# Kernel tuning notes

Hardware: AMD Instinct MI355X
Metric: run time of the kernel (lower is better)

## Reference

```python
import jax, jax.numpy as jnp
import numpy as np

N_HEADS = 8
HIDDEN = 256
D_HEAD = HIDDEN // N_HEADS
N_NODES = 4096
N_EDGES = 16384


def setup_inputs() -> dict:
    key = jax.random.key(0)
    ks = jax.random.split(key, 12)
    s = 0.05
    return {
        "q": jax.random.normal(ks[0], (N_EDGES, HIDDEN), jnp.float32),
        "k": jax.random.normal(ks[1], (N_NODES, HIDDEN), jnp.float32),
        "v": jax.random.normal(ks[2], (N_NODES, HIDDEN), jnp.float32),
        "T": jax.random.uniform(ks[3], (N_NODES, N_EDGES), jnp.float32),
        "Wq": jax.random.normal(ks[4], (HIDDEN, HIDDEN), jnp.float32) * s,
        "bq": jax.random.normal(ks[5], (HIDDEN,), jnp.float32) * s,
        "Wk": jax.random.normal(ks[6], (HIDDEN, HIDDEN), jnp.float32) * s,
        "bk": jax.random.normal(ks[7], (HIDDEN,), jnp.float32) * s,
        "Wv": jax.random.normal(ks[8], (HIDDEN, HIDDEN), jnp.float32) * s,
        "bv": jax.random.normal(ks[9], (HIDDEN,), jnp.float32) * s,
        "Wo": jax.random.normal(ks[10], (HIDDEN, HIDDEN), jnp.float32) * s,
        "bo": jax.random.normal(ks[11], (HIDDEN,), jnp.float32) * s,
    }


def reference(q, k, v, T, Wq, bq, Wk, bk, Wv, bv, Wo, bo):
    scale = D_HEAD ** (-0.5)
    # projections, reshaped to per-head layout
    qh = (q @ Wq.T + bq).reshape(-1, N_HEADS, D_HEAD)  # [E, H, d]
    kh = (k @ Wk.T + bk).reshape(-1, N_HEADS, D_HEAD)  # [N, H, d]
    vh = (v @ Wv.T + bv).reshape(-1, N_HEADS, D_HEAD)  # [N, H, d]
    # row-normalized transition matrix (rows with zero sum left unscaled)
    row_sum = jnp.sum(T, axis=-1, keepdims=True)       # [N, 1]
    Tn = T / jnp.where(row_sum == 0, 1.0, row_sum)     # [N, E]
    # edge->node aggregation of queries, then scale
    qn = jnp.einsum("ne,ehd->nhd", Tn, qh) * scale     # [N, H, d]
    # attention: full NxN scores per head
    scores = jnp.einsum("nhd,mhd->hnm", qn, kh)        # [H, N, N]
    attn = jax.nn.softmax(scores, axis=-1)
    ctx = jnp.einsum("hnm,mhd->nhd", attn, vh)         # [N, H, d]
    out = ctx.reshape(-1, N_HEADS * D_HEAD) @ Wo.T + bo  # [N, hidden]
    return out
```

## Files before the change

kernel.cpp:

```cpp
#include <hip/hip_runtime.h>


#define N_NODES 4096
#define N_EDGES 16384
#define HIDDEN  256
#define KSPLIT  16

typedef __attribute__((ext_vector_type(4))) float f32x4;
typedef __attribute__((ext_vector_type(8))) short s16x8;
typedef __attribute__((ext_vector_type(4))) unsigned short u16x4;
typedef __attribute__((ext_vector_type(8))) unsigned short u16x8;

__device__ __forceinline__ unsigned short f2bf(float f) {
    union { float f; unsigned u; } x; x.f = f;
    unsigned r = x.u + 0x7FFFu + ((x.u >> 16) & 1u);
    return (unsigned short)(r >> 16);
}
__device__ __forceinline__ s16x8 pack8s(f32x4 x, f32x4 y) {
    u16x8 o;
    o[0]=f2bf(x[0]); o[1]=f2bf(x[1]); o[2]=f2bf(x[2]); o[3]=f2bf(x[3]);
    o[4]=f2bf(y[0]); o[5]=f2bf(y[1]); o[6]=f2bf(y[2]); o[7]=f2bf(y[3]);
    union { u16x8 u; s16x8 s; } c; c.u = o; return c.s;
}

__global__ __launch_bounds__(256)
void cvtW(const float* __restrict__ Wq, const float* __restrict__ Wk,
          const float* __restrict__ Wv, const float* __restrict__ Wo,
          unsigned short* __restrict__ dst)
{
    const int g = blockIdx.x * 256 + threadIdx.x;
    const long base = (long)g * 8;
    const int mat = (int)(base >> 16), off = (int)(base & 65535);
    const float* src = (mat == 0) ? Wq : (mat == 1) ? Wk : (mat == 2) ? Wv : Wo;
    f32x4 x = *(const f32x4*)&src[off];
    f32x4 y = *(const f32x4*)&src[off + 4];
    union { u16x8 u; s16x8 s; } c; c.s = pack8s(x, y);
    *(u16x8*)&dst[base] = c.u;
}

template<int MODE>
__global__ __launch_bounds__(256)
void proj_mfma(const float* __restrict__ A, const unsigned short* __restrict__ Wbf,
               const float* __restrict__ bias, unsigned short* __restrict__ out, int M)
{
    const int t = threadIdx.x;
    const int w = t >> 6, l = t & 63, lo = l & 15, h4 = l >> 4;
    const int m0 = blockIdx.x * 64 + w * 16;
    const int bn = blockIdx.y * 64;
    const float* Ar = A + (long)(m0 + lo) * 256 + h4 * 8;

    f32x4 acc[4] = {};
    #pragma unroll
    for (int kk = 0; kk < 8; ++kk) {
        f32x4 x = *(const f32x4*)&Ar[kk * 32];
        f32x4 y = *(const f32x4*)&Ar[kk * 32 + 4];
        s16x8 af = pack8s(x, y);
        #pragma unroll
        for (int nj = 0; nj < 4; ++nj) {
            s16x8 bf = *(const s16x8*)&Wbf[(bn + nj * 16 + lo) * 256 + kk * 32 + h4 * 8];
            acc[nj] = __builtin_amdgcn_mfma_f32_16x16x32_bf16(af, bf, acc[nj], 0, 0, 0);
        }
    }
    #pragma unroll
    for (int nj = 0; nj < 4; ++nj) {
        const int n = bn + nj * 16 + lo;
        const float bi = bias[n];
        if (MODE == 1) {
            #pragma unroll
            for (int r = 0; r < 4; ++r)
                out[(long)(m0 + h4 * 4 + r) * 256 + n] = f2bf(acc[nj][r] + bi);
        } else {
            u16x4 o;
            #pragma unroll
            for (int r = 0; r < 4; ++r) o[r] = f2bf(acc[nj][r] + bi);
            *(u16x4*)&out[(long)n * M + m0 + h4 * 4] = o;
        }
    }
}

__global__ __launch_bounds__(256)
void proj_out_mfma(const float* __restrict__ pctx, const float* __restrict__ plp,
                   const unsigned short* __restrict__ Wobf, const float* __restrict__ bo,
                   float* __restrict__ out)
{
    const int t = threadIdx.x;
    const int w = t >> 6, l = t & 63, lo = l & 15, h4 = l >> 4;
    const int m0 = blockIdx.x * 64 + w * 16;
    const int bn = blockIdx.y * 64;
    const int m = m0 + lo;

    float inv[8];
    #pragma unroll
    for (int h = 0; h < 8; ++h) {
        float s = plp[(0 * 8 + h) * N_NODES + m] + plp[(1 * 8 + h) * N_NODES + m]
                + plp[(2 * 8 + h) * N_NODES + m] + plp[(3 * 8 + h) * N_NODES + m];
        inv[h] = 1.0f / s;
    }
    const float* P = pctx + (long)m * 256;
    const long PS = (long)N_NODES * 256;

    f32x4 acc[4] = {};
    #pragma unroll
    for (int kk = 0; kk < 8; ++kk) {
        const int off = kk * 32 + h4 * 8;
        f32x4 x = *(const f32x4*)&P[off]          + *(const f32x4*)&P[PS + off]
                + *(const f32x4*)&P[2 * PS + off] + *(const f32x4*)&P[3 * PS + off];
        f32x4 y = *(const f32x4*)&P[off + 4]          + *(const f32x4*)&P[PS + off + 4]
                + *(const f32x4*)&P[2 * PS + off + 4] + *(const f32x4*)&P[3 * PS + off + 4];
        s16x8 af = pack8s(x * inv[kk], y * inv[kk]);
        #pragma unroll
        for (int nj = 0; nj < 4; ++nj) {
            s16x8 bf = *(const s16x8*)&Wobf[(bn + nj * 16 + lo) * 256 + kk * 32 + h4 * 8];
            acc[nj] = __builtin_amdgcn_mfma_f32_16x16x32_bf16(af, bf, acc[nj], 0, 0, 0);
        }
    }
    #pragma unroll
    for (int nj = 0; nj < 4; ++nj) {
        const int n = bn + nj * 16 + lo;
        const float bi = bo[n];
        #pragma unroll
        for (int r = 0; r < 4; ++r)
            out[(long)(m0 + h4 * 4 + r) * 256 + n] = acc[nj][r] + bi;
    }
}

__global__ __launch_bounds__(512, 4)
void tgemm(const float* __restrict__ T, const unsigned short* __restrict__ Bt,
           float* __restrict__ part, float* __restrict__ rsp)
{
    __shared__ __align__(16) unsigned short Bsm[2][256 * 64];
    const int t  = threadIdx.x;
    const int ks = blockIdx.x & 15, ms = blockIdx.x >> 4;
    const int m0 = ms * 128;
    const long k00 = (long)ks * 1024;
    const int w = t >> 6, l = t & 63, lo = l & 15, h4 = l >> 4;

    const int kx = ((l & 7) * 8) ^ ((l >> 3) << 3);
    const unsigned short* Bsrc = Bt + k00 + kx;

#define STAGE(itv, bufv) do {                                                       \
    const unsigned short* _s = Bsrc + (long)(itv) * 64;                             \
    unsigned short* _d = &Bsm[(bufv)][w * 2048];                                    \
    _Pragma("unroll")                                                               \
    for (int _i = 0; _i < 4; ++_i)                                                  \
        __builtin_amdgcn_global_load_lds(                                           \
            (const __attribute__((address_space(1))) unsigned int*)                 \
                (_s + (long)(w * 32 + _i * 8 + (l >> 3)) * N_EDGES),                \
            (__attribute__((address_space(3))) unsigned int*)(_d + _i * 512),       \
            16, 0, 0);                                                              \
} while (0)

    const float* Arow = T + (long)(m0 + w * 16 + lo) * N_EDGES + k00 + h4 * 8;

    STAGE(0, 0);
    f32x4 a0 = *(const f32x4*)&Arow[0];
    f32x4 a1 = *(const f32x4*)&Arow[4];
    f32x4 a2 = *(const f32x4*)&Arow[32];
    f32x4 a3 = *(const f32x4*)&Arow[36];
    __syncthreads();

    f32x4 acc[16] = {};
    float rs = 0.f;

    for (int it = 0; it < 16; ++it) {
        const int cur = it & 1;
        if (it < 15) STAGE(it + 1, cur ^ 1);
        s16x8 af0 = pack8s(a0, a1);
        s16x8 af1 = pack8s(a2, a3);
        rs += a0[0]+a0[1]+a0[2]+a0[3] + a1[0]+a1[1]+a1[2]+a1[3]
            + a2[0]+a2[1]+a2[2]+a2[3] + a3[0]+a3[1]+a3[2]+a3[3];
        if (it < 15) {
            const float* An = Arow + (it + 1) * 64;
            a0 = *(const f32x4*)&An[0];
            a1 = *(const f32x4*)&An[4];
            a2 = *(const f32x4*)&An[32];
            a3 = *(const f32x4*)&An[36];
        }
        const unsigned short* Bb = Bsm[cur];
        const int swz = (lo & 7) << 3;
        #pragma unroll
        for (int nj = 0; nj < 16; ++nj) {
            const int jb = (nj * 16 + lo) * 64;
            s16x8 bf0 = *(const s16x8*)&Bb[jb + ((h4 * 8) ^ swz)];
            s16x8 bf1 = *(const s16x8*)&Bb[jb + ((32 + h4 * 8) ^ swz)];
            acc[nj] = __builtin_amdgcn_mfma_f32_16x16x32_bf16(af0, bf0, acc[nj], 0, 0, 0);
            acc[nj] = __builtin_amdgcn_mfma_f32_16x16x32_bf16(af1, bf1, acc[nj], 0, 0, 0);
        }
        __syncthreads();
    }
#undef STAGE

    rs += __shfl_xor(rs, 16); rs += __shfl_xor(rs, 32);
    if (h4 == 0) rsp[ks * N_NODES + m0 + w * 16 + lo] = rs;

    float* P = part + (long)ks * (N_NODES * HIDDEN);
    #pragma unroll
    for (int nj = 0; nj < 16; ++nj)
        #pragma unroll
        for (int r = 0; r < 4; ++r)
            P[(long)(m0 + w * 16 + h4 * 4 + r) * HIDDEN + nj * 16 + lo] = acc[nj][r];
}

__global__ __launch_bounds__(256)
void finalize(const float* __restrict__ part, const float* __restrict__ rsp,
              unsigned short* __restrict__ qn)
{
    const int idx = blockIdx.x * 256 + threadIdx.x;
    const long i4 = (long)idx * 4;
    const int n = (int)(i4 >> 8);
    f32x4 s = {};
    #pragma unroll
    for (int ksp = 0; ksp < KSPLIT; ++ksp)
        s += *(const f32x4*)&part[(long)ksp * (N_NODES * HIDDEN) + i4];
    float rs = 0.f;
    #pragma unroll
    for (int ksp = 0; ksp < KSPLIT; ++ksp) rs += rsp[ksp * N_NODES + n];
    rs = (rs == 0.0f) ? 1.0f : rs;
    const float sc = 0.17677669529663687f / rs;
    u16x4 o;
    #pragma unroll
    for (int i = 0; i < 4; ++i) o[i] = f2bf(s[i] * sc);
    *(u16x4*)&qn[i4] = o;
}

__global__ __launch_bounds__(256)
void attn(const unsigned short* __restrict__ qn, const unsigned short* __restrict__ kh,
          const unsigned short* __restrict__ vht, float* __restrict__ pctx,
          float* __restrict__ plp)
{
    __shared__ __align__(16) unsigned short Ksm[64 * 40];
    __shared__ __align__(16) unsigned short Vsm[32 * 72];
    __shared__ __align__(16) unsigned short Psm[4][32 * 72];
    const int t  = threadIdx.x;
    const int hh = blockIdx.x >> 7, nb = (blockIdx.x >> 2) & 31, mh = blockIdx.x & 3;
    const int w = t >> 6, l = t & 63, lo = l & 15, h4 = l >> 4;
    const int n0 = nb * 128 + w * 32;

    const int km = t >> 2, kdc = (t & 3) * 8;
    const int vd = t >> 3, vmc = (t & 7) * 8;

    s16x8 qf[2];
    #pragma unroll
    for (int ni = 0; ni < 2; ++ni)
        qf[ni] = *(const s16x8*)&qn[(long)(n0 + ni * 16 + lo) * HIDDEN + hh * 32 + h4 * 8];

    f32x4 acc[2][2] = {};
    float lp[2][4] = {};
    const f32x4 zero = {};

    for (int mt = mh * 16; mt < mh * 16 + 16; ++mt) {
        const int m0 = mt * 64;
        *(s16x8*)&Ksm[km * 40 + kdc] =
            *(const s16x8*)&kh[(long)(m0 + km) * HIDDEN + hh * 32 + kdc];
        *(s16x8*)&Vsm[vd * 72 + vmc] =
            *(const s16x8*)&vht[(long)(hh * 32 + vd) * N_NODES + m0 + vmc];
        __syncthreads();

        s16x8 kb[4];
        #pragma unroll
        for (int mi = 0; mi < 4; ++mi)
            kb[mi] = *(const s16x8*)&Ksm[(mi * 16 + lo) * 40 + h4 * 8];
        #pragma unroll
        for (int ni = 0; ni < 2; ++ni) {
            #pragma unroll
            for (int mi = 0; mi < 4; ++mi) {
                f32x4 s = __builtin_amdgcn_mfma_f32_16x16x32_bf16(qf[ni], kb[mi], zero, 0, 0, 0);
                #pragma unroll
                for (int r = 0; r < 4; ++r) {
                    float p = __expf(s[r]);
                    lp[ni][r] += p;
                    Psm[w][(ni * 16 + h4 * 4 + r) * 72 + mi * 16 + lo] = f2bf(p);
                }
            }
        }
        s16x8 pa[2][2], vb[2][2];
        #pragma unroll
        for (int ni = 0; ni < 2; ++ni)
            #pragma unroll
            for (int k2 = 0; k2 < 2; ++k2)
                pa[ni][k2] = *(const s16x8*)&Psm[w][(ni * 16 + lo) * 72 + k2 * 32 + h4 * 8];
        #pragma unroll
        for (int di = 0; di < 2; ++di)
            #pragma unroll
            for (int k2 = 0; k2 < 2; ++k2)
                vb[di][k2] = *(const s16x8*)&Vsm[(di * 16 + lo) * 72 + k2 * 32 + h4 * 8];
        #pragma unroll
        for (int k2 = 0; k2 < 2; ++k2)
            #pragma unroll
            for (int ni = 0; ni < 2; ++ni)
                #pragma unroll
                for (int di = 0; di < 2; ++di)
                    acc[ni][di] = __builtin_amdgcn_mfma_f32_16x16x32_bf16(
                        pa[ni][k2], vb[di][k2], acc[ni][di], 0, 0, 0);
        __syncthreads();
    }
    #pragma unroll
    for (int ni = 0; ni < 2; ++ni)
        #pragma unroll
        for (int r = 0; r < 4; ++r) {
            float v2 = lp[ni][r];
            v2 += __shfl_xor(v2, 1); v2 += __shfl_xor(v2, 2);
            v2 += __shfl_xor(v2, 4); v2 += __shfl_xor(v2, 8);
            lp[ni][r] = v2;
        }
    float* myctx = pctx + (long)mh * (N_NODES * HIDDEN);
    float* myplp = plp  + (long)(mh * 8 + hh) * N_NODES;
    if (lo == 0)
        #pragma unroll
        for (int ni = 0; ni < 2; ++ni)
            #pragma unroll
            for (int r = 0; r < 4; ++r)
                myplp[n0 + ni * 16 + h4 * 4 + r] = lp[ni][r];
    #pragma unroll
    for (int ni = 0; ni < 2; ++ni)
        #pragma unroll
        for (int di = 0; di < 2; ++di)
            #pragma unroll
            for (int r = 0; r < 4; ++r)
                myctx[(long)(n0 + ni * 16 + h4 * 4 + r) * HIDDEN + hh * 32 + di * 16 + lo]
                    = acc[ni][di][r];
}

extern "C" void kernel_launch(void* const* d_in, const int* in_sizes, int n_in,
                              void* d_out, int out_size, void* d_ws, size_t ws_size,
                              hipStream_t stream)
{
    const float* q  = (const float*)d_in[0];
    const float* k  = (const float*)d_in[1];
    const float* v  = (const float*)d_in[2];
    const float* T  = (const float*)d_in[3];
    const float* Wq = (const float*)d_in[4];  const float* bq = (const float*)d_in[5];
    const float* Wk = (const float*)d_in[6];  const float* bk = (const float*)d_in[7];
    const float* Wv = (const float*)d_in[8];  const float* bv = (const float*)d_in[9];
    const float* Wo = (const float*)d_in[10]; const float* bo = (const float*)d_in[11];

    char* w = (char*)d_ws;
    unsigned short* qh_t = (unsigned short*)(w);
    unsigned short* kh   = (unsigned short*)(w + (8u  << 20));
    unsigned short* vh_t = (unsigned short*)(w + (10u << 20));
    unsigned short* qn   = (unsigned short*)(w + (12u << 20));
    float*          pctx = (float*)         (w + (14u << 20));
    float*          plp  = (float*)         (w + (30u << 20));
    float*          part = (float*)         (w + (32u << 20));
    float*          rsp  = (float*)         (w + (96u << 20));
    unsigned short* wbf  = (unsigned short*)(w + (97u << 20));
    unsigned short* wq_bf = wbf;
    unsigned short* wk_bf = wbf + 65536;
    unsigned short* wv_bf = wbf + 2 * 65536;
    unsigned short* wo_bf = wbf + 3 * 65536;

    cvtW<<<128, 256, 0, stream>>>(Wq, Wk, Wv, Wo, wbf);
    proj_mfma<2><<<dim3(256, 4), 256, 0, stream>>>(q, wq_bf, bq, qh_t, N_EDGES);
    proj_mfma<1><<<dim3(64, 4),  256, 0, stream>>>(k, wk_bf, bk, kh,   N_NODES);
    proj_mfma<2><<<dim3(64, 4),  256, 0, stream>>>(v, wv_bf, bv, vh_t, N_NODES);
    tgemm<<<512, 512, 0, stream>>>(T, qh_t, part, rsp);
    finalize<<<1024, 256, 0, stream>>>(part, rsp, qn);
    attn<<<1024, 256, 0, stream>>>(qn, kh, vh_t, pctx, plp);
    proj_out_mfma<<<dim3(64, 4), 256, 0, stream>>>(pctx, plp, wo_bf, bo, (float*)d_out);
}
```

Measured before the change: 214.7 us.

## Double-buffer A-tile registers and replace syncthreads with split barriers and partial vmcnt waits

The T-row fragments are now held in a two-bank register array, so the loads for the next K-step are issued together with the async LDS stage of the B tile. Each iteration replaces the trailing __syncthreads with a pair of raw s_barrier calls around an explicit s_waitcnt vmcnt(8). That wait lets the current tile's loads complete while the next tile's eight loads stay in flight. The aim is to hide the global-load latency of the fp32 T stream behind the MFMA loop and to avoid the full vmcnt(0) drain that __syncthreads implies. The risks are that the dynamic a[cur] indexing may be lowered to selects or scratch, and that the compiler's own waitcnt insertion may undo the partial wait.

```diff
diff --git a/kernel.cpp b/kernel.cpp
--- a/kernel.cpp
+++ b/kernel.cpp
@@ -152,30 +152,40 @@
 
     const float* Arow = T + (long)(m0 + w * 16 + lo) * N_EDGES + k00 + h4 * 8;
 
+#define LOADA(bank, itv) do {                                                       \
+    const float* _a = Arow + (itv) * 64;                                            \
+    a[bank][0] = *(const f32x4*)&_a[0];                                             \
+    a[bank][1] = *(const f32x4*)&_a[4];                                             \
+    a[bank][2] = *(const f32x4*)&_a[32];                                            \
+    a[bank][3] = *(const f32x4*)&_a[36];                                            \
+} while (0)
+
+    f32x4 a[2][4];
     STAGE(0, 0);
-    f32x4 a0 = *(const f32x4*)&Arow[0];
-    f32x4 a1 = *(const f32x4*)&Arow[4];
-    f32x4 a2 = *(const f32x4*)&Arow[32];
-    f32x4 a3 = *(const f32x4*)&Arow[36];
-    __syncthreads();
+    LOADA(0, 0);
 
     f32x4 acc[16] = {};
     float rs = 0.f;
 
     for (int it = 0; it < 16; ++it) {
         const int cur = it & 1;
-        if (it < 15) STAGE(it + 1, cur ^ 1);
-        s16x8 af0 = pack8s(a0, a1);
-        s16x8 af1 = pack8s(a2, a3);
-        rs += a0[0]+a0[1]+a0[2]+a0[3] + a1[0]+a1[1]+a1[2]+a1[3]
-            + a2[0]+a2[1]+a2[2]+a2[3] + a3[0]+a3[1]+a3[2]+a3[3];
+        __builtin_amdgcn_s_barrier();
         if (it < 15) {
-            const float* An = Arow + (it + 1) * 64;
-            a0 = *(const f32x4*)&An[0];
-            a1 = *(const f32x4*)&An[4];
-            a2 = *(const f32x4*)&An[32];
-            a3 = *(const f32x4*)&An[36];
-        }
+            STAGE(it + 1, cur ^ 1);
+            LOADA(cur ^ 1, it + 1);
+            asm volatile("s_waitcnt vmcnt(8)" ::: "memory");
+        } else {
+            asm volatile("s_waitcnt vmcnt(0)" ::: "memory");
+        }
+        __builtin_amdgcn_s_barrier();
+
+        s16x8 af0 = pack8s(a[cur][0], a[cur][1]);
+        s16x8 af1 = pack8s(a[cur][2], a[cur][3]);
+        rs += a[cur][0][0]+a[cur][0][1]+a[cur][0][2]+a[cur][0][3]
+            + a[cur][1][0]+a[cur][1][1]+a[cur][1][2]+a[cur][1][3]
+            + a[cur][2][0]+a[cur][2][1]+a[cur][2][2]+a[cur][2][3]
+            + a[cur][3][0]+a[cur][3][1]+a[cur][3][2]+a[cur][3][3];
+
         const unsigned short* Bb = Bsm[cur];
         const int swz = (lo & 7) << 3;
         #pragma unroll
@@ -186,9 +196,9 @@
             acc[nj] = __builtin_amdgcn_mfma_f32_16x16x32_bf16(af0, bf0, acc[nj], 0, 0, 0);
             acc[nj] = __builtin_amdgcn_mfma_f32_16x16x32_bf16(af1, bf1, acc[nj], 0, 0, 0);
         }
-        __syncthreads();
     }
 #undef STAGE
+#undef LOADA
 
     rs += __shfl_xor(rs, 16); rs += __shfl_xor(rs, 32);
     if (h4 == 0) rsp[ks * N_NODES + m0 + w * 16 + lo] = rs;
```

Measured after the change: 238.1 us. +10.9%, slower.
